# Optimization experiments

Hardware: AMD Instinct MI355X
Metric: run time of the kernel (lower is better)

The kernel has to match this reference:

```python
import jax, jax.numpy as jnp
import numpy as np

N, E, DIM, HEADS, EDGE_DIM = 50000, 800000, 128, 4, 1
C = DIM // HEADS  # per-head channels
EPS = 1e-5


def graph_ln(h, w, b):
    # PyG LayerNorm, mode='graph', batch=None: normalize over ALL nodes+features
    mu = h.mean()
    hc = h - mu
    std = jnp.sqrt(jnp.mean(hc * hc))
    return hc / (std + EPS) * w + b


def setup_inputs() -> dict:
    key = jax.random.key(0)
    ks = jax.random.split(key, 16)
    s = 1.0 / np.sqrt(DIM)
    return {
        "x": jax.random.normal(ks[0], (N, DIM), jnp.float32),
        "edge_index": jax.random.randint(ks[1], (2, E), 0, N, jnp.int32),
        "edge_weight": jax.random.uniform(ks[2], (E,), jnp.float32),
        "edge_attr": jax.random.normal(ks[3], (E, EDGE_DIM), jnp.float32),
        # GCNConv params
        "W_gcn": jax.random.normal(ks[4], (DIM, DIM), jnp.float32) * s,
        "b_gcn": jnp.zeros((DIM,), jnp.float32),
        # GATv2Conv params (share_weights=True -> single lin)
        "W_l": jax.random.normal(ks[5], (DIM, DIM), jnp.float32) * s,
        "b_l": jnp.zeros((DIM,), jnp.float32),
        "W_edge": jax.random.normal(ks[6], (EDGE_DIM, DIM), jnp.float32),
        "att": jax.random.normal(ks[7], (HEADS, C), jnp.float32) * (1.0 / np.sqrt(C)),
        "b_gat": jnp.zeros((DIM,), jnp.float32),
        # norms
        "gcn_nw": jnp.ones((DIM,), jnp.float32), "gcn_nb": jnp.zeros((DIM,), jnp.float32),
        "gat_nw": jnp.ones((DIM,), jnp.float32), "gat_nb": jnp.zeros((DIM,), jnp.float32),
        "out_nw": jnp.ones((DIM,), jnp.float32), "out_nb": jnp.zeros((DIM,), jnp.float32),
        "alpha": jnp.ones((2,), jnp.float32),
    }


def reference(x, edge_index, edge_weight, edge_attr, W_gcn, b_gcn, W_l, b_l,
              W_edge, att, b_gat, gcn_nw, gcn_nb, gat_nw, gat_nb, out_nw, out_nb, alpha):
    src, dst = edge_index[0], edge_index[1]

    # ---- GCN branch (normalize=True, add_self_loops=False) ----
    deg = jax.ops.segment_sum(edge_weight, dst, num_segments=N)
    dis = jnp.where(deg > 0, jax.lax.rsqrt(jnp.maximum(deg, 1e-30)), 0.0)
    norm = dis[src] * edge_weight * dis[dst]  # [E]
    xw = x @ W_gcn  # [N, DIM]
    h = jax.ops.segment_sum(norm[:, None] * xw[src], dst, num_segments=N) + b_gcn
    gcn_out = x + jax.nn.gelu(graph_ln(h, gcn_nw, gcn_nb), approximate=False)

    # ---- GATv2 branch (share_weights=True, edge_dim=1) ----
    xl = (x @ W_l + b_l).reshape(N, HEADS, C)
    e = (edge_attr @ W_edge).reshape(E, HEADS, C)
    z = jax.nn.leaky_relu(xl[dst] + xl[src] + e, negative_slope=0.2)  # [E,H,C]
    logits = jnp.einsum('ehc,hc->eh', z, att)  # [E,H]
    m = jax.ops.segment_max(logits, dst, num_segments=N)  # [N,H]
    a = jnp.exp(logits - m[dst])
    denom = jax.ops.segment_sum(a, dst, num_segments=N)
    a = a / (denom[dst] + 1e-16)  # softmax over incoming edges per dst, per head
    msg = xl[src] * a[:, :, None]  # [E,H,C]
    g = jax.ops.segment_sum(msg, dst, num_segments=N).reshape(N, DIM) + b_gat
    gat_out = x + jax.nn.gelu(graph_ln(g, gat_nw, gat_nb), approximate=False)

    # ---- fuse ----
    w = jax.nn.softmax(alpha)
    fused = w[0] * gcn_out + w[1] * gat_out
    return jax.nn.gelu(graph_ln(fused, out_nw, out_nb), approximate=False)
```

## Files before the change

### kernel.cpp

```cpp
#include <hip/hip_runtime.h>
#include <math.h>

#define DIM 128
#define HEADS 4
#define EPS 1e-5f
#define NBLK 2048

__device__ __forceinline__ float us2f(unsigned short u) {
  union { unsigned int i; float f; } c; c.i = ((unsigned int)u) << 16; return c.f;
}
__device__ __forceinline__ unsigned short f2us(float f) {
  union { float ff; unsigned int i; } c; c.ff = f;
  return (unsigned short)((c.i + 0x7FFFu + ((c.i >> 16) & 1u)) >> 16);
}
__device__ __forceinline__ float ldf(const void* p, size_t i, int fl32) {
  return fl32 ? ((const float*)p)[i] : us2f(((const unsigned short*)p)[i]);
}
__device__ __forceinline__ float gelu_exact(float v) {
  return 0.5f * v * (1.0f + erff(v * 0.7071067811865475f));
}
__device__ __forceinline__ int imin(int a, int b) { return a < b ? a : b; }

__device__ __forceinline__ int packed_pos(int c) { return ((c & ~1) << 1) | (c & 1); }

__global__ void __launch_bounds__(256)
k_detect(const unsigned short* __restrict__ x, long n, int* __restrict__ dflag) {
  long lim = n < 8192 ? n : 8192;
  int bad = 0;
  for (long i = threadIdx.x; i < lim; i += 256) {
    float v = us2f(x[i]);
    float a = fabsf(v);
    if (!(a == 0.0f || (a > 1e-30f && a < 1e3f))) bad++;
  }
  __shared__ int sb[256];
  sb[threadIdx.x] = bad;
  __syncthreads();
  for (int off = 128; off > 0; off >>= 1) {
    if ((int)threadIdx.x < off) sb[threadIdx.x] += sb[threadIdx.x + off];
    __syncthreads();
  }
  if (threadIdx.x == 0) dflag[0] = (sb[0] > 32) ? 1 : 0;
}

__global__ void k_cnt(const int* __restrict__ dst, int* __restrict__ cnt,
                      int* __restrict__ rank, int E) {
  int e = blockIdx.x * blockDim.x + threadIdx.x;
  if (e < E) rank[e] = atomicAdd(&cnt[dst[e]], 1);
}

__global__ void __launch_bounds__(256)
k_scan(const int* __restrict__ cnt, int* __restrict__ off, int N, int E) {
  __shared__ int part[256];
  int t = threadIdx.x;
  int chunk = (N + 255) / 256;
  int lo = t * chunk;
  int hi = lo + chunk; if (hi > N) hi = N;
  int s = 0;
  for (int i = lo; i < hi; ++i) s += cnt[i];
  part[t] = s;
  __syncthreads();
  if (t == 0) {
    int run = 0;
    for (int j = 0; j < 256; ++j) { int tmp = part[j]; part[j] = run; run += tmp; }
  }
  __syncthreads();
  int run = part[t];
  for (int i = lo; i < hi; ++i) { off[i] = run; run += cnt[i]; }
  if (t == 0) off[N] = E;
}

__global__ void k_scatter(const int* __restrict__ src, const int* __restrict__ dst,
                          const void* __restrict__ ew, const void* __restrict__ ea,
                          const int* __restrict__ off, const int* __restrict__ rank,
                          int4* __restrict__ csr, int E, const int* __restrict__ df) {
  const int fl32 = *df;
  int e = blockIdx.x * blockDim.x + threadIdx.x;
  if (e >= E) return;
  int d = dst[e], s = src[e];
  int pos = off[d] + rank[e];
  float w = ldf(ew, e, fl32);
  float eav = ldf(ea, e, fl32);
  if (!isfinite(eav)) eav = 0.0f;
  csr[pos] = make_int4(s, __float_as_int(w), __float_as_int(eav), d);
}

__global__ void k_degdis(const int* __restrict__ off, const int4* __restrict__ csr,
                         float* __restrict__ dis, int N) {
  int i = blockIdx.x * blockDim.x + threadIdx.x;
  if (i >= N) return;
  int b = off[i], t = off[i + 1];
  float s = 0.f;
  for (int j = b; j < t; ++j) {
    float w = __int_as_float(csr[j].y);
    if (isfinite(w)) s += w;
  }
  dis[i] = (s > 0.0f) ? rsqrtf(fmaxf(s, 1e-30f)) : 0.0f;
}

__global__ void k_nm(int4* __restrict__ csr, const float* __restrict__ dis, int E) {
  int e = blockIdx.x * blockDim.x + threadIdx.x;
  if (e >= E) return;
  int4 c = csr[e];
  float nm = dis[c.x] * __int_as_float(c.y) * dis[c.w];
  if (!isfinite(nm)) nm = 0.0f;
  ((int*)&csr[e])[1] = __float_as_int(nm);
}

__global__ void __launch_bounds__(256)
k_wprep(const void* __restrict__ Wg, const void* __restrict__ Wl,
        const void* __restrict__ bl, unsigned short* __restrict__ Bhi,
        unsigned short* __restrict__ Blo, float* __restrict__ bias2,
        const int* __restrict__ df) {
  const int fl32 = *df;
  int g = blockIdx.x * 256 + threadIdx.x;
  int col = g >> 7, k = g & 127;
  int t4 = col >> 2, r = col & 3;
  int wcol = t4 * 2 + (r & 1);
  float v = (r < 2) ? ldf(Wl, (size_t)k * DIM + wcol, fl32)
                    : ldf(Wg, (size_t)k * DIM + wcol, fl32);
  unsigned short hi = f2us(v);
  float lo = v - us2f(hi);
  Bhi[(size_t)col * 128 + k] = hi;
  Blo[(size_t)col * 128 + k] = f2us(lo);
  if (blockIdx.x == 0) {
    int c2 = threadIdx.x;
    int tt = c2 >> 2, rr = c2 & 3;
    bias2[c2] = (rr < 2) ? ldf(bl, tt * 2 + rr, fl32) : 0.0f;
  }
}

typedef __attribute__((ext_vector_type(8))) short short8v;
typedef __attribute__((ext_vector_type(4))) float f32x4;

__global__ void __launch_bounds__(256)
k_gemm_mfma(const void* __restrict__ x, const unsigned short* __restrict__ Bhi,
            const unsigned short* __restrict__ Blo, const float* __restrict__ bias2,
            unsigned short* __restrict__ packed, int N, const int* __restrict__ df) {
  const int fl32 = *df;
  __shared__ unsigned short Ahi[64 * 128];
  __shared__ unsigned short Alo[64 * 128];
  const int tid = threadIdx.x;
  const int r0 = blockIdx.x * 64;
  #pragma unroll
  for (int it = 0; it < 8; ++it) {
    int i4 = tid + it * 256;
    int row = i4 >> 5, kq = i4 & 31;
    int grow = r0 + row;
    float v0 = 0.f, v1 = 0.f, v2 = 0.f, v3 = 0.f;
    if (grow < N) {
      if (fl32) {
        float4 f = ((const float4*)x)[(size_t)grow * 32 + kq];
        v0 = f.x; v1 = f.y; v2 = f.z; v3 = f.w;
      } else {
        ushort4 u = ((const ushort4*)x)[(size_t)grow * 32 + kq];
        v0 = us2f(u.x); v1 = us2f(u.y); v2 = us2f(u.z); v3 = us2f(u.w);
      }
    }
    ushort4 hi = make_ushort4(f2us(v0), f2us(v1), f2us(v2), f2us(v3));
    ushort4 lo = make_ushort4(f2us(v0 - us2f(hi.x)), f2us(v1 - us2f(hi.y)),
                              f2us(v2 - us2f(hi.z)), f2us(v3 - us2f(hi.w)));
    int ba = (row * 256 + kq * 8) ^ ((row & 7) << 4);
    *(ushort4*)((char*)Ahi + ba) = hi;
    *(ushort4*)((char*)Alo + ba) = lo;
  }
  __syncthreads();
  const int lane = tid & 63, wid = tid >> 6;
  const int mbase = (wid >> 1) * 32;
  const int nbase = (wid & 1) * 128;
  const int lr = lane & 15, lk = lane >> 4;
  short8v ah[2][4], al[2][4];
  #pragma unroll
  for (int m = 0; m < 2; ++m) {
    #pragma unroll
    for (int ks = 0; ks < 4; ++ks) {
      int row = mbase + m * 16 + lr;
      int ba = (row * 256 + ks * 64 + lk * 16) ^ ((row & 7) << 4);
      ah[m][ks] = *(const short8v*)((const char*)Ahi + ba);
      al[m][ks] = *(const short8v*)((const char*)Alo + ba);
    }
  }
  f32x4 acc[2][8];
  const f32x4 zero = {0.0f, 0.0f, 0.0f, 0.0f};
  #pragma unroll
  for (int m = 0; m < 2; ++m)
    #pragma unroll
    for (int n = 0; n < 8; ++n) acc[m][n] = zero;
  if (fl32) {
    #pragma unroll
    for (int n = 0; n < 8; ++n) {
      int col = nbase + n * 16 + lr;
      const unsigned short* bh0 = Bhi + (size_t)col * 128 + lk * 8;
      const unsigned short* bl0 = Blo + (size_t)col * 128 + lk * 8;
      #pragma unroll
      for (int ks = 0; ks < 4; ++ks) {
        short8v bh  = *(const short8v*)(bh0 + ks * 32);
        short8v blv = *(const short8v*)(bl0 + ks * 32);
        acc[0][n] = __builtin_amdgcn_mfma_f32_16x16x32_bf16(ah[0][ks], bh, acc[0][n], 0, 0, 0);
        acc[1][n] = __builtin_amdgcn_mfma_f32_16x16x32_bf16(ah[1][ks], bh, acc[1][n], 0, 0, 0);
        acc[0][n] = __builtin_amdgcn_mfma_f32_16x16x32_bf16(al[0][ks], bh, acc[0][n], 0, 0, 0);
        acc[1][n] = __builtin_amdgcn_mfma_f32_16x16x32_bf16(al[1][ks], bh, acc[1][n], 0, 0, 0);
        acc[0][n] = __builtin_amdgcn_mfma_f32_16x16x32_bf16(ah[0][ks], blv, acc[0][n], 0, 0, 0);
        acc[1][n] = __builtin_amdgcn_mfma_f32_16x16x32_bf16(ah[1][ks], blv, acc[1][n], 0, 0, 0);
      }
    }
  } else {
    #pragma unroll
    for (int n = 0; n < 8; ++n) {
      int col = nbase + n * 16 + lr;
      const unsigned short* bh0 = Bhi + (size_t)col * 128 + lk * 8;
      #pragma unroll
      for (int ks = 0; ks < 4; ++ks) {
        short8v bh = *(const short8v*)(bh0 + ks * 32);
        acc[0][n] = __builtin_amdgcn_mfma_f32_16x16x32_bf16(ah[0][ks], bh, acc[0][n], 0, 0, 0);
        acc[1][n] = __builtin_amdgcn_mfma_f32_16x16x32_bf16(ah[1][ks], bh, acc[1][n], 0, 0, 0);
      }
    }
  }
  #pragma unroll
  for (int m = 0; m < 2; ++m) {
    #pragma unroll
    for (int n = 0; n < 8; ++n) {
      int col = nbase + n * 16 + lr;
      float bv = bias2[col];
      int rb = r0 + mbase + m * 16 + lk * 4;
      #pragma unroll
      for (int j = 0; j < 4; ++j) {
        int row = rb + j;
        if (row < N) {
          float v = acc[m][n][j] + bv;
          if (!isfinite(v)) v = 0.0f;
          packed[(size_t)row * 256 + col] = f2us(v);
        }
      }
    }
  }
}

#define GATHER(sidx) (*(const ushort4*)(packed + (size_t)(sidx) * 256 + lane * 4))

#define PROC(v, m) {                                                       \
  float nm = __int_as_float((m).y), eav = __int_as_float((m).z);           \
  float vx = us2f((v).x), vy = us2f((v).y);                                \
  float z0 = xd0 + vx + eav * wd0; z0 = (z0 > 0.f) ? z0 : 0.2f * z0;       \
  float z1 = xd1 + vy + eav * wd1; z1 = (z1 > 0.f) ? z1 : 0.2f * z1;       \
  float dt = z0 * at0 + z1 * at1;                                          \
  dt += __shfl_xor(dt, 1);                                                 \
  dt += __shfl_xor(dt, 2);                                                 \
  dt += __shfl_xor(dt, 4);                                                 \
  dt += __shfl_xor(dt, 8);                                                 \
  float e = __expf(-fabsf(dt - mx));                                       \
  bool up = dt > mx;                                                       \
  float corr = up ? e : 1.0f;                                              \
  float w = up ? 1.0f : e;                                                 \
  mx = up ? dt : mx;                                                       \
  den = fmaf(den, corr, w);                                                \
  ga0 = fmaf(ga0, corr, w * vx);                                           \
  ga1 = fmaf(ga1, corr, w * vy);                                           \
  hc0 = fmaf(nm, us2f((v).z), hc0);                                        \
  hc1 = fmaf(nm, us2f((v).w), hc1);                                        \
}

__global__ void __launch_bounds__(256)
k_mega(const int* __restrict__ off, const int4* __restrict__ csr,
       const unsigned short* __restrict__ packed,
       const void* __restrict__ Wed, const void* __restrict__ att,
       const void* __restrict__ bgcn, const void* __restrict__ bgat,
       float* __restrict__ h, float* __restrict__ g,
       double* __restrict__ pA, double* __restrict__ pB, int N,
       const int* __restrict__ df) {
  const int fl32 = *df;
  const int wid = threadIdx.x >> 6;
  const int lane = threadIdx.x & 63;
  const int n0 = blockIdx.x * 4;
  const int node = n0 + wid;
  const int c0 = lane * 2;
  float wd0 = ldf(Wed, c0, fl32), wd1 = ldf(Wed, c0 + 1, fl32);
  float at0 = ldf(att, c0, fl32), at1 = ldf(att, c0 + 1, fl32);

  const int blkBeg = off[n0];
  const int nTop = (n0 + 4 < N) ? (n0 + 4) : N;
  const int blkEnd = off[nTop];

  int beg = 0, end = 0;
  float xd0 = 0.f, xd1 = 0.f;
  if (node < N) {
    beg = off[node]; end = off[node + 1];
    ushort4 xd = *(const ushort4*)(packed + (size_t)node * 256 + lane * 4);
    xd0 = us2f(xd.x); xd1 = us2f(xd.y);
  }
  float mx = -INFINITY, den = 0.f;
  float ga0 = 0.f, ga1 = 0.f, hc0 = 0.f, hc1 = 0.f;

  __shared__ int4 smeta[256];

  for (int base = blkBeg; base < blkEnd; base += 256) {
    int wlen = blkEnd - base; if (wlen > 256) wlen = 256;
    __syncthreads();
    if ((int)threadIdx.x < wlen) smeta[threadIdx.x] = csr[base + (int)threadIdx.x];
    __syncthreads();
    int lo = beg > base ? beg : base;
    int hiEnd = base + wlen;
    int hi = end < hiEnd ? end : hiEnd;
    int cnt = hi - lo;
    if (cnt > 0) {
      int s0 = lo - base;
      int last = s0 + cnt - 1;
      ushort4 v0, v1, v2, v3, v4, v5, v6, v7;
      v0 = GATHER(smeta[imin(s0 + 0, last)].x);
      v1 = GATHER(smeta[imin(s0 + 1, last)].x);
      v2 = GATHER(smeta[imin(s0 + 2, last)].x);
      v3 = GATHER(smeta[imin(s0 + 3, last)].x);
      v4 = GATHER(smeta[imin(s0 + 4, last)].x);
      v5 = GATHER(smeta[imin(s0 + 5, last)].x);
      v6 = GATHER(smeta[imin(s0 + 6, last)].x);
      v7 = GATHER(smeta[imin(s0 + 7, last)].x);
      int i = 0;
      for (; i + 8 <= cnt; i += 8) {
        int4 m;
        m = smeta[s0 + i + 0]; PROC(v0, m); v0 = GATHER(smeta[imin(s0 + i + 8,  last)].x);
        m = smeta[s0 + i + 1]; PROC(v1, m); v1 = GATHER(smeta[imin(s0 + i + 9,  last)].x);
        m = smeta[s0 + i + 2]; PROC(v2, m); v2 = GATHER(smeta[imin(s0 + i + 10, last)].x);
        m = smeta[s0 + i + 3]; PROC(v3, m); v3 = GATHER(smeta[imin(s0 + i + 11, last)].x);
        m = smeta[s0 + i + 4]; PROC(v4, m); v4 = GATHER(smeta[imin(s0 + i + 12, last)].x);
        m = smeta[s0 + i + 5]; PROC(v5, m); v5 = GATHER(smeta[imin(s0 + i + 13, last)].x);
        m = smeta[s0 + i + 6]; PROC(v6, m); v6 = GATHER(smeta[imin(s0 + i + 14, last)].x);
        m = smeta[s0 + i + 7]; PROC(v7, m); v7 = GATHER(smeta[imin(s0 + i + 15, last)].x);
      }
      if (i < cnt) { int4 m = smeta[s0 + i]; PROC(v0, m); ++i; }
      if (i < cnt) { int4 m = smeta[s0 + i]; PROC(v1, m); ++i; }
      if (i < cnt) { int4 m = smeta[s0 + i]; PROC(v2, m); ++i; }
      if (i < cnt) { int4 m = smeta[s0 + i]; PROC(v3, m); ++i; }
      if (i < cnt) { int4 m = smeta[s0 + i]; PROC(v4, m); ++i; }
      if (i < cnt) { int4 m = smeta[s0 + i]; PROC(v5, m); ++i; }
      if (i < cnt) { int4 m = smeta[s0 + i]; PROC(v6, m); ++i; }
    }
  }

  double sA = 0.0, sA2 = 0.0, sB = 0.0, sB2 = 0.0;
  if (node < N) {
    float inv = (end > beg) ? 1.0f / (den + 1e-16f) : 0.0f;
    ga0 *= inv; ga1 *= inv;
    if (!isfinite(ga0)) ga0 = 0.0f;
    if (!isfinite(ga1)) ga1 = 0.0f;
    if (!isfinite(hc0)) hc0 = 0.0f;
    if (!isfinite(hc1)) hc1 = 0.0f;
    *(float2*)(h + (size_t)node * DIM + c0) = make_float2(hc0, hc1);
    *(float2*)(g + (size_t)node * DIM + c0) = make_float2(ga0, ga1);
    float hA0 = hc0 + ldf(bgcn, c0, fl32), hA1 = hc1 + ldf(bgcn, c0 + 1, fl32);
    float gB0 = ga0 + ldf(bgat, c0, fl32), gB1 = ga1 + ldf(bgat, c0 + 1, fl32);
    sA  = (double)hA0 + (double)hA1;
    sA2 = (double)hA0 * hA0 + (double)hA1 * hA1;
    sB  = (double)gB0 + (double)gB1;
    sB2 = (double)gB0 * gB0 + (double)gB1 * gB1;
  }
  __shared__ double l1[256], l2[256], l3[256], l4[256];
  l1[threadIdx.x] = sA; l2[threadIdx.x] = sA2; l3[threadIdx.x] = sB; l4[threadIdx.x] = sB2;
  __syncthreads();
  for (int o = 128; o > 0; o >>= 1) {
    if ((int)threadIdx.x < o) {
      l1[threadIdx.x] += l1[threadIdx.x + o];
      l2[threadIdx.x] += l2[threadIdx.x + o];
      l3[threadIdx.x] += l3[threadIdx.x + o];
      l4[threadIdx.x] += l4[threadIdx.x + o];
    }
    __syncthreads();
  }
  if (threadIdx.x == 0) {
    pA[2 * blockIdx.x] = l1[0]; pA[2 * blockIdx.x + 1] = l2[0];
    pB[2 * blockIdx.x] = l3[0]; pB[2 * blockIdx.x + 1] = l4[0];
  }
}

__device__ __forceinline__ void ln_params(double S, double S2, double M, float* mu_out, float* sc_out) {
  double mu = S / M;
  double v = S2 / M - mu * mu;
  if (!(v > 0.0)) v = 0.0;
  float fmu = (float)mu;
  float sc = 1.0f / ((float)sqrt(v) + EPS);
  if (!isfinite(fmu)) fmu = 0.0f;
  if (!isfinite(sc)) sc = 0.0f;
  *mu_out = fmu; *sc_out = sc;
}

__global__ void __launch_bounds__(256)
k_fin12(const double* __restrict__ pA, const double* __restrict__ pB, int nblk,
        const void* __restrict__ alpha, float* __restrict__ params, double M,
        const int* __restrict__ df) {
  const int fl32 = *df;
  __shared__ double l1[256], l2[256], l3[256], l4[256];
  double a = 0, b = 0, c = 0, d = 0;
  for (int j = threadIdx.x; j < nblk; j += 256) {
    a += pA[2 * j]; b += pA[2 * j + 1];
    c += pB[2 * j]; d += pB[2 * j + 1];
  }
  l1[threadIdx.x] = a; l2[threadIdx.x] = b; l3[threadIdx.x] = c; l4[threadIdx.x] = d;
  __syncthreads();
  for (int off = 128; off > 0; off >>= 1) {
    if ((int)threadIdx.x < off) {
      l1[threadIdx.x] += l1[threadIdx.x + off];
      l2[threadIdx.x] += l2[threadIdx.x + off];
      l3[threadIdx.x] += l3[threadIdx.x + off];
      l4[threadIdx.x] += l4[threadIdx.x + off];
    }
    __syncthreads();
  }
  if (threadIdx.x == 0) {
    ln_params(l1[0], l2[0], M, &params[0], &params[1]);
    ln_params(l3[0], l4[0], M, &params[2], &params[3]);
    float a0 = ldf(alpha, 0, fl32), a1 = ldf(alpha, 1, fl32);
    if (!isfinite(a0)) a0 = 0.0f;
    if (!isfinite(a1)) a1 = 0.0f;
    float mx = fmaxf(a0, a1);
    float e0 = expf(a0 - mx), e1 = expf(a1 - mx);
    float inv = 1.0f / (e0 + e1);
    params[4] = e0 * inv;
    params[5] = e1 * inv;
  }
}

__global__ void __launch_bounds__(256)
k_fin3(const double* __restrict__ pC, float* __restrict__ params, double M) {
  __shared__ double l1[256], l2[256];
  double a = 0, b = 0;
  for (int j = threadIdx.x; j < NBLK; j += 256) { a += pC[2 * j]; b += pC[2 * j + 1]; }
  l1[threadIdx.x] = a; l2[threadIdx.x] = b;
  __syncthreads();
  for (int off = 128; off > 0; off >>= 1) {
    if ((int)threadIdx.x < off) {
      l1[threadIdx.x] += l1[threadIdx.x + off];
      l2[threadIdx.x] += l2[threadIdx.x + off];
    }
    __syncthreads();
  }
  if (threadIdx.x == 0) ln_params(l1[0], l2[0], M, &params[6], &params[7]);
}

__global__ void __launch_bounds__(256)
k_fuse(const void* __restrict__ x, float* h, const float* __restrict__ g,
       const void* __restrict__ b_gcn, const void* __restrict__ b_gat,
       const void* __restrict__ gcn_nw, const void* __restrict__ gcn_nb,
       const void* __restrict__ gat_nw, const void* __restrict__ gat_nb,
       const float* __restrict__ params, double* __restrict__ pC, long n4,
       const int* __restrict__ df) {
  const int fl32 = *df;
  float mu1 = params[0], sc1 = params[1], mu2 = params[2], sc2 = params[3];
  float w0 = params[4], w1 = params[5];
  double s = 0.0, s2 = 0.0;
  long stride = (long)gridDim.x * blockDim.x;
  for (long i4 = (long)blockIdx.x * blockDim.x + threadIdx.x; i4 < n4; i4 += stride) {
    int c = (int)((i4 * 4) & (DIM - 1));
    float4 hv4 = ((const float4*)h)[i4];
    float4 gv4 = ((const float4*)g)[i4];
    float xv[4];
    if (fl32) {
      float4 xf = ((const float4*)x)[i4];
      xv[0] = xf.x; xv[1] = xf.y; xv[2] = xf.z; xv[3] = xf.w;
    } else {
      ushort4 xu = ((const ushort4*)x)[i4];
      xv[0] = us2f(xu.x); xv[1] = us2f(xu.y); xv[2] = us2f(xu.z); xv[3] = us2f(xu.w);
    }
    float hv[4] = {hv4.x, hv4.y, hv4.z, hv4.w};
    float gv[4] = {gv4.x, gv4.y, gv4.z, gv4.w};
    float fo[4];
    #pragma unroll
    for (int j = 0; j < 4; ++j) {
      int cj = c + j;
      float hb = hv[j] + ldf(b_gcn, cj, fl32);
      float gb = gv[j] + ldf(b_gat, cj, fl32);
      float go = xv[j] + gelu_exact((hb - mu1) * sc1 * ldf(gcn_nw, cj, fl32) + ldf(gcn_nb, cj, fl32));
      float ao = xv[j] + gelu_exact((gb - mu2) * sc2 * ldf(gat_nw, cj, fl32) + ldf(gat_nb, cj, fl32));
      float f = w0 * go + w1 * ao;
      if (!isfinite(f)) f = 0.0f;
      fo[j] = f;
      s += f; s2 += (double)f * f;
    }
    ((float4*)h)[i4] = make_float4(fo[0], fo[1], fo[2], fo[3]);
  }
  __shared__ double ls[256], ls2[256];
  ls[threadIdx.x] = s; ls2[threadIdx.x] = s2;
  __syncthreads();
  for (int off = 128; off > 0; off >>= 1) {
    if ((int)threadIdx.x < off) {
      ls[threadIdx.x] += ls[threadIdx.x + off];
      ls2[threadIdx.x] += ls2[threadIdx.x + off];
    }
    __syncthreads();
  }
  if (threadIdx.x == 0) { pC[2 * blockIdx.x] = ls[0]; pC[2 * blockIdx.x + 1] = ls2[0]; }
}

__global__ void k_final(const float* __restrict__ fused, const void* __restrict__ nw,
                        const void* __restrict__ nb, const float* __restrict__ params,
                        void* __restrict__ out, long n4, const int* __restrict__ df) {
  const int fl32 = *df;
  long i4 = (long)blockIdx.x * blockDim.x + threadIdx.x;
  if (i4 >= n4) return;
  int c = (int)((i4 * 4) & (DIM - 1));
  float mu = params[6], sc = params[7];
  float4 f4 = ((const float4*)fused)[i4];
  float fv[4] = {f4.x, f4.y, f4.z, f4.w};
  float rv[4];
  #pragma unroll
  for (int j = 0; j < 4; ++j) {
    int cj = c + j;
    float r = gelu_exact((fv[j] - mu) * sc * ldf(nw, cj, fl32) + ldf(nb, cj, fl32));
    if (!isfinite(r)) r = 0.0f;
    rv[j] = r;
  }
  if (fl32) {
    ((float4*)out)[i4] = make_float4(rv[0], rv[1], rv[2], rv[3]);
  } else {
    ((ushort4*)out)[i4] = make_ushort4(f2us(rv[0]), f2us(rv[1]), f2us(rv[2]), f2us(rv[3]));
  }
}

extern "C" void kernel_launch(void* const* d_in, const int* in_sizes, int n_in,
                              void* d_out, int out_size, void* d_ws, size_t ws_size,
                              hipStream_t stream) {
  const void* x    = d_in[0];
  const int*  ei   = (const int*)d_in[1];
  const void* ew   = d_in[2];
  const void* ea   = d_in[3];
  const void* Wg   = d_in[4];
  const void* bgcn = d_in[5];
  const void* Wl   = d_in[6];
  const void* bl   = d_in[7];
  const void* Wed  = d_in[8];
  const void* att  = d_in[9];
  const void* bgat = d_in[10];
  const void* gcn_nw = d_in[11];
  const void* gcn_nb = d_in[12];
  const void* gat_nw = d_in[13];
  const void* gat_nb = d_in[14];
  const void* out_nw = d_in[15];
  const void* out_nb = d_in[16];
  const void* alpha  = d_in[17];

  const int N = in_sizes[0] / DIM;
  const int E = in_sizes[2];
  const int* src  = ei;
  const int* dstp = ei + E;
  const size_t ND = (size_t)N * DIM;
  const int nAgg = (N + 3) / 4;

  char* ws = (char*)d_ws;
  size_t o = 0;
  auto alloc = [&](size_t bytes) { size_t r = o; o += (bytes + 255) & ~(size_t)255; return r; };
  size_t o_deg    = alloc((size_t)N * 4);
  size_t o_cnt    = alloc((size_t)N * 4);
  size_t zero_end = o;
  size_t o_off    = alloc((size_t)(N + 1) * 4);
  size_t o_h      = alloc(ND * 4);
  size_t o_g      = alloc(ND * 4);
  size_t o_packed = alloc(ND * 4);
  size_t o_csr    = alloc((size_t)E * 16);
  size_t o_par    = alloc(8 * 4);
  size_t o_pA     = alloc((size_t)nAgg * 2 * 8);
  size_t o_pB     = alloc((size_t)nAgg * 2 * 8);
  size_t o_pC     = alloc((size_t)NBLK * 2 * 8);
  size_t o_flag   = alloc(4);
  size_t o_bh     = alloc((size_t)256 * 128 * 2);
  size_t o_blo    = alloc((size_t)256 * 128 * 2);
  size_t o_b2     = alloc((size_t)256 * 4);
  (void)ws_size; (void)n_in; (void)out_size;

  float* dis     = (float*)(ws + o_deg);
  int*   cnt     = (int*)(ws + o_cnt);
  int*   off     = (int*)(ws + o_off);
  float* h       = (float*)(ws + o_h);
  int*   rank    = (int*)(ws + o_h);
  float* g       = (float*)(ws + o_g);
  unsigned short* packed = (unsigned short*)(ws + o_packed);
  int4*  csr     = (int4*)(ws + o_csr);
  float* params  = (float*)(ws + o_par);
  double* pA     = (double*)(ws + o_pA);
  double* pB     = (double*)(ws + o_pB);
  double* pC     = (double*)(ws + o_pC);
  int* dflag     = (int*)(ws + o_flag);
  unsigned short* Bhi = (unsigned short*)(ws + o_bh);
  unsigned short* Blo = (unsigned short*)(ws + o_blo);
  float* bias2   = (float*)(ws + o_b2);

  hipMemsetAsync(ws, 0, zero_end, stream);
  k_detect<<<1, 256, 0, stream>>>((const unsigned short*)x, (long)ND, dflag);

  k_wprep<<<128, 256, 0, stream>>>(Wg, Wl, bl, Bhi, Blo, bias2, dflag);

  int ebk = (E + 255) / 256;
  k_cnt<<<ebk, 256, 0, stream>>>(dstp, cnt, rank, E);
  k_scan<<<1, 256, 0, stream>>>(cnt, off, N, E);
  k_scatter<<<ebk, 256, 0, stream>>>(src, dstp, ew, ea, off, rank, csr, E, dflag);
  k_degdis<<<(N + 255) / 256, 256, 0, stream>>>(off, csr, dis, N);
  k_nm<<<ebk, 256, 0, stream>>>(csr, dis, E);

  k_gemm_mfma<<<(N + 63) / 64, 256, 0, stream>>>(x, Bhi, Blo, bias2, packed, N, dflag);

  k_mega<<<nAgg, 256, 0, stream>>>(off, csr, packed, Wed, att, bgcn, bgat,
                                   h, g, pA, pB, N, dflag);

  k_fin12<<<1, 256, 0, stream>>>(pA, pB, nAgg, alpha, params, (double)ND, dflag);

  const long n4 = (long)(ND / 4);
  k_fuse<<<NBLK, 256, 0, stream>>>(x, h, g, bgcn, bgat, gcn_nw, gcn_nb, gat_nw, gat_nb,
                                   params, pC, n4, dflag);
  k_fin3<<<1, 256, 0, stream>>>(pC, params, (double)ND);
  k_final<<<(int)((n4 + 255) / 256), 256, 0, stream>>>(h, out_nw, out_nb, params,
                                                       d_out, n4, dflag);
}
```

Before: 510.3 us.

## Merge small setup kernels and fold final reduction into fuse via last-block pattern

Cuts the launch count by combining independent kernels into single grids with block-index dispatch: detect with count, scan with weight prep (using 1024-thread blocks and a parallel Hillis-Steele scan), and degree/dis with the GEMM. The separate final-stats reduction kernel is replaced by a last-block-done atomic counter inside the fuse kernel. The bf16 input path no longer builds or loads the unused low-part tile. The aim is to remove per-launch overhead and serialization bubbles between tiny kernels. The cost is more complex kernels and reliance on threadfence/atomic ordering.

```diff
diff --git a/kernel.cpp b/kernel.cpp
--- a/kernel.cpp
+++ b/kernel.cpp
@@ -21,52 +21,73 @@
 }
 __device__ __forceinline__ int imin(int a, int b) { return a < b ? a : b; }
 
-__device__ __forceinline__ int packed_pos(int c) { return ((c & ~1) << 1) | (c & 1); }
-
 __global__ void __launch_bounds__(256)
-k_detect(const unsigned short* __restrict__ x, long n, int* __restrict__ dflag) {
-  long lim = n < 8192 ? n : 8192;
-  int bad = 0;
-  for (long i = threadIdx.x; i < lim; i += 256) {
-    float v = us2f(x[i]);
-    float a = fabsf(v);
-    if (!(a == 0.0f || (a > 1e-30f && a < 1e3f))) bad++;
-  }
-  __shared__ int sb[256];
-  sb[threadIdx.x] = bad;
-  __syncthreads();
-  for (int off = 128; off > 0; off >>= 1) {
-    if ((int)threadIdx.x < off) sb[threadIdx.x] += sb[threadIdx.x + off];
-    __syncthreads();
-  }
-  if (threadIdx.x == 0) dflag[0] = (sb[0] > 32) ? 1 : 0;
-}
-
-__global__ void k_cnt(const int* __restrict__ dst, int* __restrict__ cnt,
-                      int* __restrict__ rank, int E) {
-  int e = blockIdx.x * blockDim.x + threadIdx.x;
-  if (e < E) rank[e] = atomicAdd(&cnt[dst[e]], 1);
-}
-
-__global__ void __launch_bounds__(256)
-k_scan(const int* __restrict__ cnt, int* __restrict__ off, int N, int E) {
-  __shared__ int part[256];
-  int t = threadIdx.x;
-  int chunk = (N + 255) / 256;
-  int lo = t * chunk;
-  int hi = lo + chunk; if (hi > N) hi = N;
-  int s = 0;
-  for (int i = lo; i < hi; ++i) s += cnt[i];
-  part[t] = s;
-  __syncthreads();
-  if (t == 0) {
-    int run = 0;
-    for (int j = 0; j < 256; ++j) { int tmp = part[j]; part[j] = run; run += tmp; }
-  }
-  __syncthreads();
-  int run = part[t];
-  for (int i = lo; i < hi; ++i) { off[i] = run; run += cnt[i]; }
-  if (t == 0) off[N] = E;
+k_fa(const unsigned short* __restrict__ x, long n, int* __restrict__ dflag,
+     const int* __restrict__ dst, int* __restrict__ cnt, int* __restrict__ rank, int E) {
+  if (blockIdx.x == 0) {
+    long lim = n < 8192 ? n : 8192;
+    int bad = 0;
+    for (long i = threadIdx.x; i < lim; i += 256) {
+      float v = us2f(x[i]);
+      float a = fabsf(v);
+      if (!(a == 0.0f || (a > 1e-30f && a < 1e3f))) bad++;
+    }
+    __shared__ int sb[256];
+    sb[threadIdx.x] = bad;
+    __syncthreads();
+    for (int off = 128; off > 0; off >>= 1) {
+      if ((int)threadIdx.x < off) sb[threadIdx.x] += sb[threadIdx.x + off];
+      __syncthreads();
+    }
+    if (threadIdx.x == 0) dflag[0] = (sb[0] > 32) ? 1 : 0;
+  } else {
+    int e = (blockIdx.x - 1) * 256 + threadIdx.x;
+    if (e < E) rank[e] = atomicAdd(&cnt[dst[e]], 1);
+  }
+}
+
+__global__ void __launch_bounds__(1024)
+k_fb(const int* __restrict__ cnt, int* __restrict__ off, int N, int E,
+     const void* __restrict__ Wg, const void* __restrict__ Wl,
+     const void* __restrict__ bl, unsigned short* __restrict__ Bhi,
+     unsigned short* __restrict__ Blo, float* __restrict__ bias2,
+     const int* __restrict__ df) {
+  if (blockIdx.x == 0) {
+    __shared__ int part[1024];
+    int t = threadIdx.x;
+    int chunk = (N + 1023) / 1024;
+    int lo = t * chunk;
+    int hi = lo + chunk; if (hi > N) hi = N;
+    int s = 0;
+    for (int i = lo; i < hi; ++i) s += cnt[i];
+    part[t] = s;
+    __syncthreads();
+    for (int o = 1; o < 1024; o <<= 1) {
+      int v = (t >= o) ? part[t - o] : 0;
+      __syncthreads();
+      part[t] += v;
+      __syncthreads();
+    }
+    int run = (t == 0) ? 0 : part[t - 1];
+    for (int i = lo; i < hi; ++i) { off[i] = run; run += cnt[i]; }
+    if (t == 0) off[N] = E;
+  } else {
+    const int fl32 = *df;
+    int g = (blockIdx.x - 1) * 1024 + threadIdx.x;
+    int col = g >> 7, k = g & 127;
+    int t4 = col >> 2, r = col & 3;
+    int wcol = t4 * 2 + (r & 1);
+    float v = (r < 2) ? ldf(Wl, (size_t)k * DIM + wcol, fl32)
+                      : ldf(Wg, (size_t)k * DIM + wcol, fl32);
+    unsigned short hi = f2us(v);
+    float lo = v - us2f(hi);
+    Bhi[(size_t)col * 128 + k] = hi;
+    Blo[(size_t)col * 128 + k] = f2us(lo);
+    if (g < 256) {
+      int tt = g >> 2, rr = g & 3;
+      bias2[g] = (rr < 2) ? ldf(bl, tt * 2 + rr, fl32) : 0.0f;
+    }
+  }
 }
 
 __global__ void k_scatter(const int* __restrict__ src, const int* __restrict__ dst,
@@ -84,19 +105,6 @@
   csr[pos] = make_int4(s, __float_as_int(w), __float_as_int(eav), d);
 }
 
-__global__ void k_degdis(const int* __restrict__ off, const int4* __restrict__ csr,
-                         float* __restrict__ dis, int N) {
-  int i = blockIdx.x * blockDim.x + threadIdx.x;
-  if (i >= N) return;
-  int b = off[i], t = off[i + 1];
-  float s = 0.f;
-  for (int j = b; j < t; ++j) {
-    float w = __int_as_float(csr[j].y);
-    if (isfinite(w)) s += w;
-  }
-  dis[i] = (s > 0.0f) ? rsqrtf(fmaxf(s, 1e-30f)) : 0.0f;
-}
-
 __global__ void k_nm(int4* __restrict__ csr, const float* __restrict__ dis, int E) {
   int e = blockIdx.x * blockDim.x + threadIdx.x;
   if (e >= E) return;
@@ -106,69 +114,69 @@
   ((int*)&csr[e])[1] = __float_as_int(nm);
 }
 
-__global__ void __launch_bounds__(256)
-k_wprep(const void* __restrict__ Wg, const void* __restrict__ Wl,
-        const void* __restrict__ bl, unsigned short* __restrict__ Bhi,
-        unsigned short* __restrict__ Blo, float* __restrict__ bias2,
-        const int* __restrict__ df) {
-  const int fl32 = *df;
-  int g = blockIdx.x * 256 + threadIdx.x;
-  int col = g >> 7, k = g & 127;
-  int t4 = col >> 2, r = col & 3;
-  int wcol = t4 * 2 + (r & 1);
-  float v = (r < 2) ? ldf(Wl, (size_t)k * DIM + wcol, fl32)
-                    : ldf(Wg, (size_t)k * DIM + wcol, fl32);
-  unsigned short hi = f2us(v);
-  float lo = v - us2f(hi);
-  Bhi[(size_t)col * 128 + k] = hi;
-  Blo[(size_t)col * 128 + k] = f2us(lo);
-  if (blockIdx.x == 0) {
-    int c2 = threadIdx.x;
-    int tt = c2 >> 2, rr = c2 & 3;
-    bias2[c2] = (rr < 2) ? ldf(bl, tt * 2 + rr, fl32) : 0.0f;
-  }
-}
-
 typedef __attribute__((ext_vector_type(8))) short short8v;
 typedef __attribute__((ext_vector_type(4))) float f32x4;
 
 __global__ void __launch_bounds__(256)
-k_gemm_mfma(const void* __restrict__ x, const unsigned short* __restrict__ Bhi,
-            const unsigned short* __restrict__ Blo, const float* __restrict__ bias2,
-            unsigned short* __restrict__ packed, int N, const int* __restrict__ df) {
+k_fd(const void* __restrict__ x, const unsigned short* __restrict__ Bhi,
+     const unsigned short* __restrict__ Blo, const float* __restrict__ bias2,
+     unsigned short* __restrict__ packed, int N, const int* __restrict__ df,
+     const int* __restrict__ off, const int4* __restrict__ csr,
+     float* __restrict__ dis, int gemmBlocks) {
   const int fl32 = *df;
+  if ((int)blockIdx.x >= gemmBlocks) {
+    int i = ((int)blockIdx.x - gemmBlocks) * 256 + threadIdx.x;
+    if (i < N) {
+      int b = off[i], t = off[i + 1];
+      float s = 0.f;
+      for (int j = b; j < t; ++j) {
+        float w = __int_as_float(csr[j].y);
+        if (isfinite(w)) s += w;
+      }
+      dis[i] = (s > 0.0f) ? rsqrtf(fmaxf(s, 1e-30f)) : 0.0f;
+    }
+    return;
+  }
   __shared__ unsigned short Ahi[64 * 128];
   __shared__ unsigned short Alo[64 * 128];
   const int tid = threadIdx.x;
   const int r0 = blockIdx.x * 64;
-  #pragma unroll
-  for (int it = 0; it < 8; ++it) {
-    int i4 = tid + it * 256;
-    int row = i4 >> 5, kq = i4 & 31;
-    int grow = r0 + row;
-    float v0 = 0.f, v1 = 0.f, v2 = 0.f, v3 = 0.f;
-    if (grow < N) {
-      if (fl32) {
+  if (fl32) {
+    #pragma unroll
+    for (int it = 0; it < 8; ++it) {
+      int i4 = tid + it * 256;
+      int row = i4 >> 5, kq = i4 & 31;
+      int grow = r0 + row;
+      float v0 = 0.f, v1 = 0.f, v2 = 0.f, v3 = 0.f;
+      if (grow < N) {
         float4 f = ((const float4*)x)[(size_t)grow * 32 + kq];
         v0 = f.x; v1 = f.y; v2 = f.z; v3 = f.w;
-      } else {
-        ushort4 u = ((const ushort4*)x)[(size_t)grow * 32 + kq];
-        v0 = us2f(u.x); v1 = us2f(u.y); v2 = us2f(u.z); v3 = us2f(u.w);
-      }
-    }
-    ushort4 hi = make_ushort4(f2us(v0), f2us(v1), f2us(v2), f2us(v3));
-    ushort4 lo = make_ushort4(f2us(v0 - us2f(hi.x)), f2us(v1 - us2f(hi.y)),
-                              f2us(v2 - us2f(hi.z)), f2us(v3 - us2f(hi.w)));
-    int ba = (row * 256 + kq * 8) ^ ((row & 7) << 4);
-    *(ushort4*)((char*)Ahi + ba) = hi;
-    *(ushort4*)((char*)Alo + ba) = lo;
+      }
+      ushort4 hi = make_ushort4(f2us(v0), f2us(v1), f2us(v2), f2us(v3));
+      ushort4 lo = make_ushort4(f2us(v0 - us2f(hi.x)), f2us(v1 - us2f(hi.y)),
+                                f2us(v2 - us2f(hi.z)), f2us(v3 - us2f(hi.w)));
+      int ba = (row * 256 + kq * 8) ^ ((row & 7) << 4);
+      *(ushort4*)((char*)Ahi + ba) = hi;
+      *(ushort4*)((char*)Alo + ba) = lo;
+    }
+  } else {
+    #pragma unroll
+    for (int it = 0; it < 8; ++it) {
+      int i4 = tid + it * 256;
+      int row = i4 >> 5, kq = i4 & 31;
+      int grow = r0 + row;
+      ushort4 hi = make_ushort4(0, 0, 0, 0);
+      if (grow < N) hi = ((const ushort4*)x)[(size_t)grow * 32 + kq];
+      int ba = (row * 256 + kq * 8) ^ ((row & 7) << 4);
+      *(ushort4*)((char*)Ahi + ba) = hi;
+    }
   }
   __syncthreads();
   const int lane = tid & 63, wid = tid >> 6;
   const int mbase = (wid >> 1) * 32;
   const int nbase = (wid & 1) * 128;
   const int lr = lane & 15, lk = lane >> 4;
-  short8v ah[2][4], al[2][4];
+  short8v ah[2][4];
   #pragma unroll
   for (int m = 0; m < 2; ++m) {
     #pragma unroll
@@ -176,7 +184,6 @@
       int row = mbase + m * 16 + lr;
       int ba = (row * 256 + ks * 64 + lk * 16) ^ ((row & 7) << 4);
       ah[m][ks] = *(const short8v*)((const char*)Ahi + ba);
-      al[m][ks] = *(const short8v*)((const char*)Alo + ba);
     }
   }
   f32x4 acc[2][8];
@@ -186,6 +193,16 @@
     #pragma unroll
     for (int n = 0; n < 8; ++n) acc[m][n] = zero;
   if (fl32) {
+    short8v al[2][4];
+    #pragma unroll
+    for (int m = 0; m < 2; ++m) {
+      #pragma unroll
+      for (int ks = 0; ks < 4; ++ks) {
+        int row = mbase + m * 16 + lr;
+        int ba = (row * 256 + ks * 64 + lk * 16) ^ ((row & 7) << 4);
+        al[m][ks] = *(const short8v*)((const char*)Alo + ba);
+      }
+    }
     #pragma unroll
     for (int n = 0; n < 8; ++n) {
       int col = nbase + n * 16 + lr;
@@ -419,28 +436,12 @@
 }
 
 __global__ void __launch_bounds__(256)
-k_fin3(const double* __restrict__ pC, float* __restrict__ params, double M) {
-  __shared__ double l1[256], l2[256];
-  double a = 0, b = 0;
-  for (int j = threadIdx.x; j < NBLK; j += 256) { a += pC[2 * j]; b += pC[2 * j + 1]; }
-  l1[threadIdx.x] = a; l2[threadIdx.x] = b;
-  __syncthreads();
-  for (int off = 128; off > 0; off >>= 1) {
-    if ((int)threadIdx.x < off) {
-      l1[threadIdx.x] += l1[threadIdx.x + off];
-      l2[threadIdx.x] += l2[threadIdx.x + off];
-    }
-    __syncthreads();
-  }
-  if (threadIdx.x == 0) ln_params(l1[0], l2[0], M, &params[6], &params[7]);
-}
-
-__global__ void __launch_bounds__(256)
 k_fuse(const void* __restrict__ x, float* h, const float* __restrict__ g,
        const void* __restrict__ b_gcn, const void* __restrict__ b_gat,
        const void* __restrict__ gcn_nw, const void* __restrict__ gcn_nb,
        const void* __restrict__ gat_nw, const void* __restrict__ gat_nb,
-       const float* __restrict__ params, double* __restrict__ pC, long n4,
+       float* __restrict__ params, double* __restrict__ pC,
+       unsigned int* __restrict__ fcnt, long n4, double M,
        const int* __restrict__ df) {
   const int fl32 = *df;
   float mu1 = params[0], sc1 = params[1], mu2 = params[2], sc2 = params[3];
@@ -477,6 +478,7 @@
     ((float4*)h)[i4] = make_float4(fo[0], fo[1], fo[2], fo[3]);
   }
   __shared__ double ls[256], ls2[256];
+  __shared__ bool slast;
   ls[threadIdx.x] = s; ls2[threadIdx.x] = s2;
   __syncthreads();
   for (int off = 128; off > 0; off >>= 1) {
@@ -486,7 +488,30 @@
     }
     __syncthreads();
   }
-  if (threadIdx.x == 0) { pC[2 * blockIdx.x] = ls[0]; pC[2 * blockIdx.x + 1] = ls2[0]; }
+  if (threadIdx.x == 0) {
+    pC[2 * blockIdx.x] = ls[0]; pC[2 * blockIdx.x + 1] = ls2[0];
+    __threadfence();
+    unsigned int old = atomicAdd(fcnt, 1u);
+    slast = (old == (unsigned int)(gridDim.x - 1));
+  }
+  __syncthreads();
+  if (slast) {
+    __threadfence();
+    double a = 0, b = 0;
+    for (int j = threadIdx.x; j < (int)gridDim.x; j += 256) {
+      a += pC[2 * j]; b += pC[2 * j + 1];
+    }
+    ls[threadIdx.x] = a; ls2[threadIdx.x] = b;
+    __syncthreads();
+    for (int off = 128; off > 0; off >>= 1) {
+      if ((int)threadIdx.x < off) {
+        ls[threadIdx.x] += ls[threadIdx.x + off];
+        ls2[threadIdx.x] += ls2[threadIdx.x + off];
+      }
+      __syncthreads();
+    }
+    if (threadIdx.x == 0) ln_params(ls[0], ls2[0], M, &params[6], &params[7]);
+  }
 }
 
 __global__ void k_final(const float* __restrict__ fused, const void* __restrict__ nw,
@@ -548,6 +573,7 @@
   auto alloc = [&](size_t bytes) { size_t r = o; o += (bytes + 255) & ~(size_t)255; return r; };
   size_t o_deg    = alloc((size_t)N * 4);
   size_t o_cnt    = alloc((size_t)N * 4);
+  size_t o_fcnt   = alloc(4);
   size_t zero_end = o;
   size_t o_off    = alloc((size_t)(N + 1) * 4);
   size_t o_h      = alloc(ND * 4);
@@ -566,6 +592,7 @@
 
   float* dis     = (float*)(ws + o_deg);
   int*   cnt     = (int*)(ws + o_cnt);
+  unsigned int* fcnt = (unsigned int*)(ws + o_fcnt);
   int*   off     = (int*)(ws + o_off);
   float* h       = (float*)(ws + o_h);
   int*   rank    = (int*)(ws + o_h);
@@ -582,18 +609,20 @@
   float* bias2   = (float*)(ws + o_b2);
 
   hipMemsetAsync(ws, 0, zero_end, stream);
-  k_detect<<<1, 256, 0, stream>>>((const unsigned short*)x, (long)ND, dflag);
-
-  k_wprep<<<128, 256, 0, stream>>>(Wg, Wl, bl, Bhi, Blo, bias2, dflag);
 
   int ebk = (E + 255) / 256;
-  k_cnt<<<ebk, 256, 0, stream>>>(dstp, cnt, rank, E);
-  k_scan<<<1, 256, 0, stream>>>(cnt, off, N, E);
+  k_fa<<<1 + ebk, 256, 0, stream>>>((const unsigned short*)x, (long)ND, dflag,
+                                    dstp, cnt, rank, E);
+  k_fb<<<33, 1024, 0, stream>>>(cnt, off, N, E, Wg, Wl, bl, Bhi, Blo, bias2, dflag);
+
   k_scatter<<<ebk, 256, 0, stream>>>(src, dstp, ew, ea, off, rank, csr, E, dflag);
-  k_degdis<<<(N + 255) / 256, 256, 0, stream>>>(off, csr, dis, N);
+
+  const int gemmBlocks = (N + 63) / 64;
+  const int degBlocks = (N + 255) / 256;
+  k_fd<<<gemmBlocks + degBlocks, 256, 0, stream>>>(x, Bhi, Blo, bias2, packed, N, dflag,
+                                                   off, csr, dis, gemmBlocks);
+
   k_nm<<<ebk, 256, 0, stream>>>(csr, dis, E);
-
-  k_gemm_mfma<<<(N + 63) / 64, 256, 0, stream>>>(x, Bhi, Blo, bias2, packed, N, dflag);
 
   k_mega<<<nAgg, 256, 0, stream>>>(off, csr, packed, Wed, att, bgcn, bgat,
                                    h, g, pA, pB, N, dflag);
@@ -602,8 +631,7 @@
 
   const long n4 = (long)(ND / 4);
   k_fuse<<<NBLK, 256, 0, stream>>>(x, h, g, bgcn, bgat, gcn_nw, gcn_nb, gat_nw, gat_nb,
-                                   params, pC, n4, dflag);
-  k_fin3<<<1, 256, 0, stream>>>(pC, params, (double)ND);
+                                   params, pC, fcnt, n4, (double)ND, dflag);
   k_final<<<(int)((n4 + 255) / 256), 256, 0, stream>>>(h, out_nw, out_nb, params,
                                                        d_out, n4, dflag);
 }
```

Measured after the change: 530.5 us. 1.04x slower.
